# Performance work log

Hardware: AMD Instinct MI355X
Metric: run time of the kernel (lower is better)

The kernel has to match this reference:

```python
import jax, jax.numpy as jnp
import numpy as np

HIDDEN = 1024
HEADS = 16
DK = HIDDEN // HEADS  # 64
B, N = 2, 2048


def setup_inputs() -> dict:
    key = jax.random.key(0)
    ks = jax.random.split(key, 12)
    s = 0.02
    return {
        "q": jax.random.normal(ks[0], (B, N, HIDDEN), jnp.float32),
        "k": jax.random.normal(ks[1], (B, N, HIDDEN), jnp.float32),
        "v": jax.random.normal(ks[2], (B, N, HIDDEN), jnp.float32),
        "attn_bias": jax.random.normal(ks[3], (B, N, N), jnp.float32),
        "attention_mask": jnp.zeros((B, N, N), jnp.float32),
        # projection weights stored [in, out]
        "Wq": jax.random.normal(ks[4], (HIDDEN, HIDDEN), jnp.float32) * s,
        "bq": jnp.zeros((HIDDEN,), jnp.float32),
        "Wk": jax.random.normal(ks[5], (HIDDEN, HIDDEN), jnp.float32) * s,
        "bk": jnp.zeros((HIDDEN,), jnp.float32),
        "Wv": jax.random.normal(ks[6], (HIDDEN, HIDDEN), jnp.float32) * s,
        "bv": jnp.zeros((HIDDEN,), jnp.float32),
        "Wo": jax.random.normal(ks[7], (HIDDEN, HIDDEN), jnp.float32) * s,
        "bo": jnp.zeros((HIDDEN,), jnp.float32),
    }


def reference(q, k, v, attn_bias, attention_mask, Wq, bq, Wk, bk, Wv, bv, Wo, bo):
    b, n, _ = q.shape
    scale = DK ** (-0.5)
    # project and split heads: [B, H, N, Dk]
    qh = (q @ Wq + bq).reshape(b, n, HEADS, DK).transpose(0, 2, 1, 3)
    kh = (k @ Wk + bk).reshape(b, -1, HEADS, DK).transpose(0, 2, 1, 3)
    vh = (v @ Wv + bv).reshape(b, -1, HEADS, DK).transpose(0, 2, 1, 3)
    # scaled scores + additive bias/mask broadcast over heads: [B, H, N, N]
    scores = jnp.einsum('bhnd,bhmd->bhnm', qh * scale, kh)
    scores = scores + attn_bias[:, None, :, :] + attention_mask[:, None, :, :]
    probs = jax.nn.softmax(scores, axis=-1)  # dropout is identity at inference
    ctx = jnp.einsum('bhnm,bhmd->bhnd', probs, vh)
    ctx = ctx.transpose(0, 2, 1, 3).reshape(b, n, HEADS * DK)
    return ctx @ Wo + bo
```

## Files before the change

kernel.cpp:

```cpp
#include <hip/hip_runtime.h>
#include <hip/hip_bf16.h>

#define HIDDEN 1024
#define NHEADS 16
#define DKH   64
#define BATCH 2
#define SEQ   2048
#define MTOT  (BATCH*SEQ)

using bf16x8 = __attribute__((ext_vector_type(8))) short;
using f32x4  = __attribute__((ext_vector_type(4))) float;
using u16x4  = __attribute__((ext_vector_type(4))) unsigned short;

__device__ __forceinline__ unsigned short f2bf(float f) {
    union { __hip_bfloat16 h; unsigned short u; } v;
    v.h = __float2bfloat16(f);
    return v.u;
}

__device__ __forceinline__ float asfloat(unsigned int u) {
    union { unsigned int u; float f; } v; v.u = u; return v.f;
}

__device__ __forceinline__ float fexp2(float x) {
#if __has_builtin(__builtin_amdgcn_exp2f)
    return __builtin_amdgcn_exp2f(x);
#else
    return exp2f(x);
#endif
}

__device__ __forceinline__ void gload16(const unsigned short* g, unsigned short* l) {
    __builtin_amdgcn_global_load_lds((const __attribute__((address_space(1))) void*)g,
                                     (__attribute__((address_space(3))) void*)l, 16, 0, 0);
}

#define L2E 1.44269504088896340736f

__global__ __launch_bounds__(256) void cvt_qkv(const float4* __restrict__ q,
                                               const float4* __restrict__ k,
                                               const float4* __restrict__ v,
                                               u16x4* __restrict__ out) {
    int i = blockIdx.x * 256 + threadIdx.x;
    const int per = MTOT * HIDDEN / 4;
    const float4* src; int t;
    if (i < per)            { src = q; t = 0; }
    else if (i < 2 * per)   { src = k; t = 1; }
    else                    { src = v; t = 2; }
    float4 f = src[i - t * per];
    u16x4 o; o.x = f2bf(f.x); o.y = f2bf(f.y); o.z = f2bf(f.z); o.w = f2bf(f.w);
    out[i] = o;
}

__global__ __launch_bounds__(256) void cvt_w(const float* __restrict__ Wq,
                                             const float* __restrict__ Wk,
                                             const float* __restrict__ Wv,
                                             const float* __restrict__ Wo,
                                             unsigned short* __restrict__ wt) {
    __shared__ float tile[64][65];
    const float* W = (blockIdx.z == 0) ? Wq : (blockIdx.z == 1) ? Wk : (blockIdx.z == 2) ? Wv : Wo;
    unsigned short* out = wt + (size_t)blockIdx.z * HIDDEN * HIDDEN;
    int kb = blockIdx.x * 64, nb = blockIdx.y * 64;
    int t = threadIdx.x;
    #pragma unroll
    for (int i = 0; i < 16; i++) {
        int idx = i * 256 + t; int r = idx >> 6, c = idx & 63;
        tile[r][c] = W[(size_t)(kb + r) * HIDDEN + nb + c];
    }
    __syncthreads();
    #pragma unroll
    for (int i = 0; i < 16; i++) {
        int idx = i * 256 + t; int n = idx >> 6, kk = idx & 63;
        out[(size_t)(nb + n) * HIDDEN + kb + kk] = f2bf(tile[kk][n]);
    }
}

__global__ __launch_bounds__(256) void combine_bias_t(const float* __restrict__ bias,
                                                      const float* __restrict__ mask,
                                                      unsigned short* __restrict__ out) {
    const int kvb = blockIdx.x, qt = blockIdx.y, b = blockIdx.z;
    const int t = threadIdx.x;
    const int q = t >> 2, kvc = (t & 3) * 8;
    const float* bp = bias + ((size_t)b * SEQ + qt * 64 + q) * SEQ + kvb * 32 + kvc;
    const float* mp = mask + ((size_t)b * SEQ + qt * 64 + q) * SEQ + kvb * 32 + kvc;
    float4 b0 = *(const float4*)bp, b1 = *(const float4*)(bp + 4);
    float4 m0 = *(const float4*)mp, m1 = *(const float4*)(mp + 4);
    union { bf16x8 v; __hip_bfloat162 hh[4]; } o;
    o.hh[0] = __float22bfloat162_rn(make_float2((b0.x + m0.x) * L2E, (b0.y + m0.y) * L2E));
    o.hh[1] = __float22bfloat162_rn(make_float2((b0.z + m0.z) * L2E, (b0.w + m0.w) * L2E));
    o.hh[2] = __float22bfloat162_rn(make_float2((b1.x + m1.x) * L2E, (b1.y + m1.y) * L2E));
    o.hh[3] = __float22bfloat162_rn(make_float2((b1.z + m1.z) * L2E, (b1.w + m1.w) * L2E));
    *(bf16x8*)(out + ((size_t)(b * 32 + qt) * 64 + kvb) * 2048 + t * 8) = o.v;
}

__device__ __forceinline__ void gemm_core_128(const unsigned short* __restrict__ X,
                                              const unsigned short* __restrict__ Wt,
                                              unsigned short* smem,
                                              int mbase, int nbase, f32x4 acc[4][4]) {
    const int tid = threadIdx.x, w = tid >> 6, ln = tid & 63;
    const int qr = (w >> 1) * 64, qc = (w & 1) * 64;
    const int g = ln >> 4, c16 = ln & 15;
    #pragma unroll
    for (int rt = 0; rt < 4; rt++)
        #pragma unroll
        for (int ct = 0; ct < 4; ct++) acc[rt][ct] = (f32x4){0.f, 0.f, 0.f, 0.f};

    for (int kk = 0; kk < HIDDEN; kk += 64) {
        __syncthreads();
        #pragma unroll
        for (int pass = 0; pass < 4; pass++) {
            int L = pass * 256 + tid;
            int r = L >> 3, c = (L & 7) ^ (r & 7);
            gload16(X  + (size_t)(mbase + r) * HIDDEN + kk + c * 8,
                    smem + (size_t)(pass * 256 + w * 64) * 8);
            gload16(Wt + (size_t)(nbase + r) * HIDDEN + kk + c * 8,
                    smem + 8192 + (size_t)(pass * 256 + w * 64) * 8);
        }
        __syncthreads();
        #pragma unroll
        for (int ks = 0; ks < 2; ks++) {
            bf16x8 af[4], bfr[4];
            #pragma unroll
            for (int rt = 0; rt < 4; rt++) {
                int r = qr + rt * 16 + c16;
                int ch = (g + ks * 4) ^ (r & 7);
                af[rt] = *(const bf16x8*)(smem + (size_t)(r * 8 + ch) * 8);
            }
            #pragma unroll
            for (int ct = 0; ct < 4; ct++) {
                int n = qc + ct * 16 + c16;
                int ch = (g + ks * 4) ^ (n & 7);
                bfr[ct] = *(const bf16x8*)(smem + 8192 + (size_t)(n * 8 + ch) * 8);
            }
            #pragma unroll
            for (int rt = 0; rt < 4; rt++)
                #pragma unroll
                for (int ct = 0; ct < 4; ct++)
                    acc[rt][ct] = __builtin_amdgcn_mfma_f32_16x16x32_bf16(af[rt], bfr[ct], acc[rt][ct], 0, 0, 0);
        }
    }
    __syncthreads();
}

__global__ __launch_bounds__(256, 2) void proj_gemm(const unsigned short* __restrict__ Xall,
                                                    const unsigned short* __restrict__ Wtall,
                                                    const float* __restrict__ bq,
                                                    const float* __restrict__ bk,
                                                    const float* __restrict__ bv,
                                                    unsigned short* __restrict__ qh,
                                                    unsigned short* __restrict__ khp,
                                                    unsigned short* __restrict__ vtt) {
    __shared__ __align__(16) unsigned short smem[18432];
    const int z = blockIdx.z;
    const unsigned short* X  = Xall  + (size_t)z * MTOT * HIDDEN;
    const unsigned short* Wt = Wtall + (size_t)z * HIDDEN * HIDDEN;
    const float* bias = (z == 0) ? bq : (z == 1) ? bk : bv;
    const int mbase = blockIdx.x * 128, nbase = blockIdx.y * 128;
    const int tid = threadIdx.x, w = tid >> 6, ln = tid & 63;
    const int qr = (w >> 1) * 64, qc = (w & 1) * 64;
    const int g = ln >> 4, c16 = ln & 15;

    f32x4 acc[4][4];
    gemm_core_128(X, Wt, smem, mbase, nbase, acc);

    const float scale = (z == 0) ? (0.125f * L2E) : 1.0f;
    float bias_v[4];
    #pragma unroll
    for (int ct = 0; ct < 4; ct++) bias_v[ct] = bias[nbase + qc + ct * 16 + c16];

    unsigned short* eld = smem + w * 4608;
    #pragma unroll
    for (int rt = 0; rt < 4; rt++)
        #pragma unroll
        for (int ct = 0; ct < 4; ct++)
            #pragma unroll
            for (int r4 = 0; r4 < 4; r4++) {
                int row_l = rt * 16 + g * 4 + r4;
                int col_l = ct * 16 + c16;
                float val = (acc[rt][ct][r4] + bias_v[ct]) * scale;
                if (z == 2) eld[col_l * 72 + row_l] = f2bf(val);
                else        eld[row_l * 72 + col_l] = f2bf(val);
            }
    __syncthreads();

    const int b = mbase >> 11;
    const int pos0 = (mbase & 2047) + qr;
    const int h = (nbase + qc) >> 6;
    const int bh = b * NHEADS + h;
    if (z == 0) {
        const int row8 = ln >> 3, col8 = (ln & 7) * 8;
        unsigned short* dst0 = qh + ((size_t)bh * SEQ + pos0) * DKH;
        #pragma unroll
        for (int j = 0; j < 8; j++) {
            int row = j * 8 + row8;
            *(bf16x8*)(dst0 + row * 64 + col8) = *(const bf16x8*)&eld[row * 72 + col8];
        }
    } else if (z == 1) {
        unsigned short* base = khp + ((size_t)bh * 64 + (pos0 >> 5)) * 2048;
        const int x = ln >> 2;
        #pragma unroll
        for (int j = 0; j < 8; j++) {
            int kvl  = (x >> 2) * 8 + (j & 1) * 4 + (x & 3);
            int row  = (j >> 2) * 32 + kvl;
            int dcol = ((j >> 1) & 1) * 32 + (ln & 3) * 8;
            *(bf16x8*)(base + j * 512 + ln * 8) = *(const bf16x8*)&eld[row * 72 + dcol];
        }
    } else {
        unsigned short* base = vtt + ((size_t)bh * 64 + (pos0 >> 5)) * 2048;
        #pragma unroll
        for (int j = 0; j < 8; j++) {
            int o = j * 512 + ln * 8;
            int tloc = o >> 11;
            int dl = (o & 2047) >> 5;
            int kvo = (ln & 3) * 8;
            *(bf16x8*)(base + o) = *(const bf16x8*)&eld[dl * 72 + tloc * 32 + kvo];
        }
    }
}

__global__ __launch_bounds__(256, 4) void attn(const unsigned short* __restrict__ qh,
                                               const unsigned short* __restrict__ khp,
                                               const unsigned short* __restrict__ vtt,
                                               const unsigned short* __restrict__ biasc,
                                               unsigned short* __restrict__ ctx) {
    __shared__ __align__(16) float red[2][2048];
    __shared__ float lred[2][32];
    __shared__ __align__(16) unsigned short tr[2][32][72];
    const int tid = threadIdx.x;
    const int w = tid >> 6, ln = tid & 63;
    const int quad = ln >> 4, c16 = ln & 15;
    const int qg = w & 1, kg = w >> 1;
    const int bid = blockIdx.x;
    const int xcd = bid & 7, s = bid >> 3;
    const int pair = xcd * 8 + (s >> 4);
    const int h = s & 15;
    const int b = pair >> 5, qt = pair & 31;
    const int bh = b * NHEADS + h;

    bf16x8 qf[2][2];
    #pragma unroll
    for (int qsub = 0; qsub < 2; qsub++) {
        const unsigned short* qp = qh + ((size_t)bh * SEQ + qt * 64 + qg * 32 + qsub * 16 + c16) * DKH + quad * 8;
        qf[qsub][0] = *(const bf16x8*)qp;
        qf[qsub][1] = *(const bf16x8*)(qp + 32);
    }

    const unsigned short* kbase = khp + (size_t)bh * 64 * 2048 + kg * 32 * 2048;
    const unsigned short* vbase = vtt + (size_t)bh * 64 * 2048 + kg * 32 * 2048;
    const unsigned short* bbase = biasc + (size_t)(b * 32 + qt) * 64 * 2048
                                + kg * 32 * 2048 + qg * 32 * 32;

    f32x4 accv[4][2];
    #pragma unroll
    for (int dt = 0; dt < 4; dt++)
        #pragma unroll
        for (int qsub = 0; qsub < 2; qsub++) accv[dt][qsub] = (f32x4){0.f, 0.f, 0.f, 0.f};
    float lacc[2] = {0.f, 0.f};

    const int lofsK = c16 * 32 + quad * 8;
    for (int j = 0; j < 32; j++) {
        const unsigned short* kt_ = kbase + j * 2048;
        const unsigned short* vt_ = vbase + j * 2048;
        const unsigned short* bt_ = bbase + j * 2048;

        bf16x8 kf[2][2];
        #pragma unroll
        for (int ks = 0; ks < 2; ks++)
            #pragma unroll
            for (int kvs = 0; kvs < 2; kvs++)
                kf[ks][kvs] = *(const bf16x8*)(kt_ + ks * 1024 + kvs * 512 + lofsK);
        bf16x8 vf[4];
        #pragma unroll
        for (int dt = 0; dt < 4; dt++)
            vf[dt] = *(const bf16x8*)(vt_ + (dt * 16 + c16) * 32 + quad * 8);
        bf16x8 braw[2];
        #pragma unroll
        for (int qsub = 0; qsub < 2; qsub++)
            braw[qsub] = *(const bf16x8*)(bt_ + (qsub * 16 + c16) * 32 + quad * 8);

        #pragma unroll
        for (int qsub = 0; qsub < 2; qsub++) {
            const unsigned int* bd = (const unsigned int*)&braw[qsub];
            f32x4 s0, s1;
            s0[0] = asfloat(bd[0] << 16); s0[1] = asfloat(bd[0] & 0xFFFF0000u);
            s0[2] = asfloat(bd[1] << 16); s0[3] = asfloat(bd[1] & 0xFFFF0000u);
            s1[0] = asfloat(bd[2] << 16); s1[1] = asfloat(bd[2] & 0xFFFF0000u);
            s1[2] = asfloat(bd[3] << 16); s1[3] = asfloat(bd[3] & 0xFFFF0000u);
            s0 = __builtin_amdgcn_mfma_f32_16x16x32_bf16(kf[0][0], qf[qsub][0], s0, 0, 0, 0);
            s0 = __builtin_amdgcn_mfma_f32_16x16x32_bf16(kf[1][0], qf[qsub][1], s0, 0, 0, 0);
            s1 = __builtin_amdgcn_mfma_f32_16x16x32_bf16(kf[0][1], qf[qsub][0], s1, 0, 0, 0);
            s1 = __builtin_amdgcn_mfma_f32_16x16x32_bf16(kf[1][1], qf[qsub][1], s1, 0, 0, 0);
            #pragma unroll
            for (int r = 0; r < 4; r++) { s0[r] = fexp2(s0[r]); s1[r] = fexp2(s1[r]); }
            lacc[qsub] += ((s0[0] + s0[1]) + (s0[2] + s0[3]))
                        + ((s1[0] + s1[1]) + (s1[2] + s1[3]));
            union { bf16x8 v; __hip_bfloat162 hh[4]; } pu;
            pu.hh[0] = __float22bfloat162_rn(make_float2(s0[0], s0[1]));
            pu.hh[1] = __float22bfloat162_rn(make_float2(s0[2], s0[3]));
            pu.hh[2] = __float22bfloat162_rn(make_float2(s1[0], s1[1]));
            pu.hh[3] = __float22bfloat162_rn(make_float2(s1[2], s1[3]));
            #pragma unroll
            for (int dt = 0; dt < 4; dt++)
                accv[dt][qsub] = __builtin_amdgcn_mfma_f32_16x16x32_bf16(vf[dt], pu.v, accv[dt][qsub], 0, 0, 0);
        }
    }

    if (kg == 1) {
        float* dst = red[qg];
        #pragma unroll
        for (int dt = 0; dt < 4; dt++)
            #pragma unroll
            for (int qsub = 0; qsub < 2; qsub++)
                *(f32x4*)(dst + (dt * 2 + qsub) * 256 + ln * 4) = accv[dt][qsub];
        #pragma unroll
        for (int qsub = 0; qsub < 2; qsub++) {
            float l = lacc[qsub];
            l += __shfl_xor(l, 16);
            l += __shfl_xor(l, 32);
            if (quad == 0) lred[qg][qsub * 16 + c16] = l;
        }
    }
    __syncthreads();
    if (kg == 0) {
        float inv[2];
        #pragma unroll
        for (int qsub = 0; qsub < 2; qsub++) {
            float l = lacc[qsub];
            l += __shfl_xor(l, 16);
            l += __shfl_xor(l, 32);
            l += lred[qg][qsub * 16 + c16];
            inv[qsub] = 1.0f / l;
        }
        #pragma unroll
        for (int dt = 0; dt < 4; dt++)
            #pragma unroll
            for (int qsub = 0; qsub < 2; qsub++) {
                accv[dt][qsub] += *(const f32x4*)(red[qg] + (dt * 2 + qsub) * 256 + ln * 4);
                #pragma unroll
                for (int r = 0; r < 4; r += 2) {
                    union { __hip_bfloat162 hh; unsigned int u; } pk;
                    pk.hh = __float22bfloat162_rn(make_float2(accv[dt][qsub][r] * inv[qsub],
                                                             accv[dt][qsub][r + 1] * inv[qsub]));
                    *(unsigned int*)&tr[qg][qsub * 16 + c16][dt * 16 + quad * 4 + r] = pk.u;
                }
            }
    }
    __syncthreads();
    if (kg == 0) {
        int q = ln >> 1, dc = (ln & 1) * 32;
        const unsigned short* srcp = &tr[qg][q][dc];
        unsigned short* dstp = ctx + ((size_t)b * SEQ + qt * 64 + qg * 32 + q) * HIDDEN + h * 64 + dc;
        *(bf16x8*)dstp        = *(const bf16x8*)srcp;
        *(bf16x8*)(dstp + 8)  = *(const bf16x8*)(srcp + 8);
        *(bf16x8*)(dstp + 16) = *(const bf16x8*)(srcp + 16);
        *(bf16x8*)(dstp + 24) = *(const bf16x8*)(srcp + 24);
    }
}

__global__ __launch_bounds__(256, 2) void outproj(const unsigned short* __restrict__ X,
                                                  const unsigned short* __restrict__ Wt,
                                                  const float* __restrict__ bo,
                                                  float* __restrict__ out) {
    __shared__ __align__(16) unsigned short smem[16384];
    const int mbase = blockIdx.x * 128, nbase = blockIdx.y * 128;
    const int tid = threadIdx.x, w = tid >> 6, ln = tid & 63;
    const int qr = (w >> 1) * 64, qc = (w & 1) * 64;
    const int g = ln >> 4, c16 = ln & 15;

    f32x4 acc[4][4];
    gemm_core_128(X, Wt, smem, mbase, nbase, acc);

    float bo_v[4];
    #pragma unroll
    for (int ct = 0; ct < 4; ct++) bo_v[ct] = bo[nbase + qc + ct * 16 + c16];
    #pragma unroll
    for (int rt = 0; rt < 4; rt++)
        #pragma unroll
        for (int ct = 0; ct < 4; ct++)
            #pragma unroll
            for (int r4 = 0; r4 < 4; r4++)
                out[(size_t)(mbase + qr + rt * 16 + g * 4 + r4) * HIDDEN + nbase + qc + ct * 16 + c16]
                    = acc[rt][ct][r4] + bo_v[ct];
}

extern "C" void kernel_launch(void* const* d_in, const int* in_sizes, int n_in,
                              void* d_out, int out_size, void* d_ws, size_t ws_size,
                              hipStream_t stream) {
    const float* q    = (const float*)d_in[0];
    const float* k    = (const float*)d_in[1];
    const float* v    = (const float*)d_in[2];
    const float* bias = (const float*)d_in[3];
    const float* mask = (const float*)d_in[4];
    const float* Wq   = (const float*)d_in[5];
    const float* bq   = (const float*)d_in[6];
    const float* Wk   = (const float*)d_in[7];
    const float* bk   = (const float*)d_in[8];
    const float* Wv   = (const float*)d_in[9];
    const float* bv   = (const float*)d_in[10];
    const float* Wo   = (const float*)d_in[11];
    const float* bo   = (const float*)d_in[12];

    char* ws = (char*)d_ws;
    unsigned short* qkv_bf = (unsigned short*)(ws);
    unsigned short* wt     = (unsigned short*)(ws + 25165824);
    unsigned short* qh     = (unsigned short*)(ws + 33554432);
    unsigned short* khp    = (unsigned short*)(ws + 41943040);
    unsigned short* vtt    = (unsigned short*)(ws + 50331648);
    unsigned short* ctx    = (unsigned short*)(ws + 58720256);
    unsigned short* biasc  = (unsigned short*)(ws + 67108864);

    cvt_qkv<<<12288, 256, 0, stream>>>((const float4*)q, (const float4*)k, (const float4*)v,
                                       (u16x4*)qkv_bf);
    cvt_w<<<dim3(16, 16, 4), 256, 0, stream>>>(Wq, Wk, Wv, Wo, wt);
    combine_bias_t<<<dim3(64, 32, 2), 256, 0, stream>>>(bias, mask, biasc);
    proj_gemm<<<dim3(32, 8, 3), 256, 0, stream>>>(qkv_bf, wt, bq, bk, bv, qh, khp, vtt);
    attn<<<1024, 256, 0, stream>>>(qh, khp, vtt, biasc, ctx);
    outproj<<<dim3(32, 8), 256, 0, stream>>>(ctx, wt + (size_t)3 * HIDDEN * HIDDEN, bo,
                                             (float*)d_out);
}
```

Measured before the change: 317.0 us.

## Fuse prep kernels and restructure attention to share K/V tiles via LDS

Merges the three conversion kernels (qkv cast, weight transpose, bias+mask combine) into one prep launch, which removes launch gaps. Attention now uses 512 blocks of 128 query rows, with each of four waves owning 32 rows over the full KV range. The blocks stage K/V tiles into LDS with global_load_lds, so all four waves reuse each tile instead of each loading it from global memory. The split-KV cross-wave reduction goes away, bias loads are prefetched one tile ahead, and the K/V/bias layouts are reworked to match. In exchange, occupancy drops to 2 blocks per CU, there are two barriers per tile, and the grid has fewer blocks.

```diff
diff --git a/kernel.cpp b/kernel.cpp
--- a/kernel.cpp
+++ b/kernel.cpp
@@ -37,60 +37,66 @@
 
 #define L2E 1.44269504088896340736f
 
-__global__ __launch_bounds__(256) void cvt_qkv(const float4* __restrict__ q,
-                                               const float4* __restrict__ k,
-                                               const float4* __restrict__ v,
-                                               u16x4* __restrict__ out) {
-    int i = blockIdx.x * 256 + threadIdx.x;
-    const int per = MTOT * HIDDEN / 4;
-    const float4* src; int t;
-    if (i < per)            { src = q; t = 0; }
-    else if (i < 2 * per)   { src = k; t = 1; }
-    else                    { src = v; t = 2; }
-    float4 f = src[i - t * per];
-    u16x4 o; o.x = f2bf(f.x); o.y = f2bf(f.y); o.z = f2bf(f.z); o.w = f2bf(f.w);
-    out[i] = o;
-}
-
-__global__ __launch_bounds__(256) void cvt_w(const float* __restrict__ Wq,
-                                             const float* __restrict__ Wk,
-                                             const float* __restrict__ Wv,
-                                             const float* __restrict__ Wo,
-                                             unsigned short* __restrict__ wt) {
+__global__ __launch_bounds__(256) void prep(const float4* __restrict__ q,
+                                            const float4* __restrict__ k,
+                                            const float4* __restrict__ v,
+                                            u16x4* __restrict__ qkv_bf,
+                                            const float* __restrict__ Wq,
+                                            const float* __restrict__ Wk,
+                                            const float* __restrict__ Wv,
+                                            const float* __restrict__ Wo,
+                                            unsigned short* __restrict__ wt,
+                                            const float* __restrict__ bias,
+                                            const float* __restrict__ mask,
+                                            unsigned short* __restrict__ biasf) {
     __shared__ float tile[64][65];
-    const float* W = (blockIdx.z == 0) ? Wq : (blockIdx.z == 1) ? Wk : (blockIdx.z == 2) ? Wv : Wo;
-    unsigned short* out = wt + (size_t)blockIdx.z * HIDDEN * HIDDEN;
-    int kb = blockIdx.x * 64, nb = blockIdx.y * 64;
-    int t = threadIdx.x;
-    #pragma unroll
-    for (int i = 0; i < 16; i++) {
-        int idx = i * 256 + t; int r = idx >> 6, c = idx & 63;
-        tile[r][c] = W[(size_t)(kb + r) * HIDDEN + nb + c];
-    }
-    __syncthreads();
-    #pragma unroll
-    for (int i = 0; i < 16; i++) {
-        int idx = i * 256 + t; int n = idx >> 6, kk = idx & 63;
-        out[(size_t)(nb + n) * HIDDEN + kb + kk] = f2bf(tile[kk][n]);
-    }
-}
-
-__global__ __launch_bounds__(256) void combine_bias_t(const float* __restrict__ bias,
-                                                      const float* __restrict__ mask,
-                                                      unsigned short* __restrict__ out) {
-    const int kvb = blockIdx.x, qt = blockIdx.y, b = blockIdx.z;
-    const int t = threadIdx.x;
-    const int q = t >> 2, kvc = (t & 3) * 8;
-    const float* bp = bias + ((size_t)b * SEQ + qt * 64 + q) * SEQ + kvb * 32 + kvc;
-    const float* mp = mask + ((size_t)b * SEQ + qt * 64 + q) * SEQ + kvb * 32 + kvc;
-    float4 b0 = *(const float4*)bp, b1 = *(const float4*)(bp + 4);
-    float4 m0 = *(const float4*)mp, m1 = *(const float4*)(mp + 4);
-    union { bf16x8 v; __hip_bfloat162 hh[4]; } o;
-    o.hh[0] = __float22bfloat162_rn(make_float2((b0.x + m0.x) * L2E, (b0.y + m0.y) * L2E));
-    o.hh[1] = __float22bfloat162_rn(make_float2((b0.z + m0.z) * L2E, (b0.w + m0.w) * L2E));
-    o.hh[2] = __float22bfloat162_rn(make_float2((b1.x + m1.x) * L2E, (b1.y + m1.y) * L2E));
-    o.hh[3] = __float22bfloat162_rn(make_float2((b1.z + m1.z) * L2E, (b1.w + m1.w) * L2E));
-    *(bf16x8*)(out + ((size_t)(b * 32 + qt) * 64 + kvb) * 2048 + t * 8) = o.v;
+    const int bid = blockIdx.x, t = threadIdx.x;
+    if (bid < 12288) {
+        int i = bid * 256 + t;
+        const int per = MTOT * HIDDEN / 4;
+        const float4* src; int tt;
+        if (i < per)            { src = q; tt = 0; }
+        else if (i < 2 * per)   { src = k; tt = 1; }
+        else                    { src = v; tt = 2; }
+        float4 f = src[i - tt * per];
+        u16x4 o; o.x = f2bf(f.x); o.y = f2bf(f.y); o.z = f2bf(f.z); o.w = f2bf(f.w);
+        qkv_bf[i] = o;
+    } else if (bid < 13312) {
+        int r = bid - 12288;
+        const int z = r >> 8; r &= 255;
+        const int kb = (r >> 4) * 64, nb = (r & 15) * 64;
+        const float* W = (z == 0) ? Wq : (z == 1) ? Wk : (z == 2) ? Wv : Wo;
+        unsigned short* out = wt + (size_t)z * HIDDEN * HIDDEN;
+        #pragma unroll
+        for (int i = 0; i < 16; i++) {
+            int idx = i * 256 + t; int rr = idx >> 6, c = idx & 63;
+            tile[rr][c] = W[(size_t)(kb + rr) * HIDDEN + nb + c];
+        }
+        __syncthreads();
+        #pragma unroll
+        for (int i = 0; i < 16; i++) {
+            int idx = i * 256 + t; int n = idx >> 6, kk = idx & 63;
+            out[(size_t)(nb + n) * HIDDEN + kb + kk] = f2bf(tile[kk][n]);
+        }
+    } else {
+        const int cb = bid - 13312;
+        const int tblk = cb & 15, g = (cb >> 4) & 127, b = cb >> 11;
+        const int tsub = t >> 6, ln = t & 63;
+        const int c16 = ln & 15, quad = ln >> 4;
+        const int tt_ = tblk * 4 + tsub;
+        const int qq = g * 16 + c16;
+        const int kv0 = tt_ * 32 + quad * 8;
+        const float* bp = bias + ((size_t)b * SEQ + qq) * SEQ + kv0;
+        const float* mp = mask + ((size_t)b * SEQ + qq) * SEQ + kv0;
+        float4 b0 = *(const float4*)bp, b1 = *(const float4*)(bp + 4);
+        float4 m0 = *(const float4*)mp, m1 = *(const float4*)(mp + 4);
+        union { bf16x8 v; __hip_bfloat162 hh[4]; } o;
+        o.hh[0] = __float22bfloat162_rn(make_float2((b0.x + m0.x) * L2E, (b0.y + m0.y) * L2E));
+        o.hh[1] = __float22bfloat162_rn(make_float2((b0.z + m0.z) * L2E, (b0.w + m0.w) * L2E));
+        o.hh[2] = __float22bfloat162_rn(make_float2((b1.x + m1.x) * L2E, (b1.y + m1.y) * L2E));
+        o.hh[3] = __float22bfloat162_rn(make_float2((b1.z + m1.z) * L2E, (b1.w + m1.w) * L2E));
+        *(bf16x8*)(biasf + (((size_t)b * 128 + g) * 64 + tt_) * 512 + ln * 8) = o.v;
+    }
 }
 
 __device__ __forceinline__ void gemm_core_128(const unsigned short* __restrict__ X,
@@ -148,8 +154,8 @@
                                                     const float* __restrict__ bk,
                                                     const float* __restrict__ bv,
                                                     unsigned short* __restrict__ qh,
-                                                    unsigned short* __restrict__ khp,
-                                                    unsigned short* __restrict__ vtt) {
+                                                    unsigned short* __restrict__ khs,
+                                                    unsigned short* __restrict__ vts) {
     __shared__ __align__(16) unsigned short smem[18432];
     const int z = blockIdx.z;
     const unsigned short* X  = Xall  + (size_t)z * MTOT * HIDDEN;
@@ -196,59 +202,52 @@
             *(bf16x8*)(dst0 + row * 64 + col8) = *(const bf16x8*)&eld[row * 72 + col8];
         }
     } else if (z == 1) {
-        unsigned short* base = khp + ((size_t)bh * 64 + (pos0 >> 5)) * 2048;
-        const int x = ln >> 2;
+        unsigned short* base = khs + ((size_t)bh * 64 + (pos0 >> 5)) * 2048;
+        const int kvp = (c16 >> 2) * 8 + (c16 & 3);
         #pragma unroll
         for (int j = 0; j < 8; j++) {
-            int kvl  = (x >> 2) * 8 + (j & 1) * 4 + (x & 3);
-            int row  = (j >> 2) * 32 + kvl;
-            int dcol = ((j >> 1) & 1) * 32 + (ln & 3) * 8;
-            *(bf16x8*)(base + j * 512 + ln * 8) = *(const bf16x8*)&eld[row * 72 + dcol];
+            int tloc = j >> 2, ks = (j >> 1) & 1, kvs = j & 1;
+            int kvl = tloc * 32 + kvp + kvs * 4;
+            *(bf16x8*)(base + tloc * 2048 + ks * 1024 + kvs * 512 + ln * 8)
+                = *(const bf16x8*)&eld[kvl * 72 + ks * 32 + g * 8];
         }
     } else {
-        unsigned short* base = vtt + ((size_t)bh * 64 + (pos0 >> 5)) * 2048;
+        unsigned short* base = vts + ((size_t)bh * 64 + (pos0 >> 5)) * 2048;
         #pragma unroll
         for (int j = 0; j < 8; j++) {
-            int o = j * 512 + ln * 8;
-            int tloc = o >> 11;
-            int dl = (o & 2047) >> 5;
-            int kvo = (ln & 3) * 8;
-            *(bf16x8*)(base + o) = *(const bf16x8*)&eld[dl * 72 + tloc * 32 + kvo];
-        }
-    }
-}
-
-__global__ __launch_bounds__(256, 4) void attn(const unsigned short* __restrict__ qh,
-                                               const unsigned short* __restrict__ khp,
-                                               const unsigned short* __restrict__ vtt,
-                                               const unsigned short* __restrict__ biasc,
+            int tloc = j >> 2, dt = j & 3;
+            *(bf16x8*)(base + tloc * 2048 + dt * 512 + ln * 8)
+                = *(const bf16x8*)&eld[(dt * 16 + c16) * 72 + tloc * 32 + g * 8];
+        }
+    }
+}
+
+__global__ __launch_bounds__(256, 2) void attn(const unsigned short* __restrict__ qh,
+                                               const unsigned short* __restrict__ khs,
+                                               const unsigned short* __restrict__ vts,
+                                               const unsigned short* __restrict__ biasf,
                                                unsigned short* __restrict__ ctx) {
-    __shared__ __align__(16) float red[2][2048];
-    __shared__ float lred[2][32];
-    __shared__ __align__(16) unsigned short tr[2][32][72];
-    const int tid = threadIdx.x;
-    const int w = tid >> 6, ln = tid & 63;
+    __shared__ __align__(16) unsigned short smem[16384];
+    const int tid = threadIdx.x, w = tid >> 6, ln = tid & 63;
     const int quad = ln >> 4, c16 = ln & 15;
-    const int qg = w & 1, kg = w >> 1;
     const int bid = blockIdx.x;
-    const int xcd = bid & 7, s = bid >> 3;
-    const int pair = xcd * 8 + (s >> 4);
-    const int h = s & 15;
-    const int b = pair >> 5, qt = pair & 31;
-    const int bh = b * NHEADS + h;
+    const int xcd = bid & 7, jj = bid >> 3;
+    const int bh = xcd * 4 + (jj >> 4);
+    const int qb = jj & 15;
+    const int b = bh >> 4, h = bh & 15;
 
     bf16x8 qf[2][2];
     #pragma unroll
     for (int qsub = 0; qsub < 2; qsub++) {
-        const unsigned short* qp = qh + ((size_t)bh * SEQ + qt * 64 + qg * 32 + qsub * 16 + c16) * DKH + quad * 8;
+        const unsigned short* qp = qh + ((size_t)bh * SEQ + qb * 128 + w * 32 + qsub * 16 + c16) * DKH + quad * 8;
         qf[qsub][0] = *(const bf16x8*)qp;
         qf[qsub][1] = *(const bf16x8*)(qp + 32);
     }
 
-    const unsigned short* kbase = khp + (size_t)bh * 64 * 2048 + kg * 32 * 2048;
-    const unsigned short* vbase = vtt + (size_t)bh * 64 * 2048 + kg * 32 * 2048;
-    const unsigned short* bbase = biasc + (size_t)(b * 32 + qt) * 64 * 2048
-                                + kg * 32 * 2048 + qg * 32 * 32;
+    const unsigned short* kT = khs + (size_t)bh * 131072;
+    const unsigned short* vT = vts + (size_t)bh * 131072;
+    const unsigned short* bb0 = biasf + (((size_t)b * 128 + qb * 8 + w * 2) * 64) * 512 + ln * 8;
+    const unsigned short* bb1 = bb0 + 32768;
 
     f32x4 accv[4][2];
     #pragma unroll
@@ -257,104 +256,104 @@
         for (int qsub = 0; qsub < 2; qsub++) accv[dt][qsub] = (f32x4){0.f, 0.f, 0.f, 0.f};
     float lacc[2] = {0.f, 0.f};
 
-    const int lofsK = c16 * 32 + quad * 8;
-    for (int j = 0; j < 32; j++) {
-        const unsigned short* kt_ = kbase + j * 2048;
-        const unsigned short* vt_ = vbase + j * 2048;
-        const unsigned short* bt_ = bbase + j * 2048;
-
-        bf16x8 kf[2][2];
-        #pragma unroll
-        for (int ks = 0; ks < 2; ks++)
-            #pragma unroll
-            for (int kvs = 0; kvs < 2; kvs++)
-                kf[ks][kvs] = *(const bf16x8*)(kt_ + ks * 1024 + kvs * 512 + lofsK);
-        bf16x8 vf[4];
-        #pragma unroll
-        for (int dt = 0; dt < 4; dt++)
-            vf[dt] = *(const bf16x8*)(vt_ + (dt * 16 + c16) * 32 + quad * 8);
-        bf16x8 braw[2];
+    bf16x8 bcur[2][4];
+    #pragma unroll
+    for (int j = 0; j < 4; j++) {
+        bcur[0][j] = *(const bf16x8*)(bb0 + j * 512);
+        bcur[1][j] = *(const bf16x8*)(bb1 + j * 512);
+    }
+
+    for (int T = 0; T < 16; T++) {
+        __syncthreads();
+        {
+            const unsigned short* ksrc = kT + T * 8192 + w * 512 + ln * 8;
+            const unsigned short* vsrc = vT + T * 8192 + w * 512 + ln * 8;
+            unsigned short* lk = smem + w * 512;
+            unsigned short* lv = smem + 8192 + w * 512;
+            #pragma unroll
+            for (int p = 0; p < 4; p++) {
+                gload16(ksrc + p * 2048, lk + p * 2048);
+                gload16(vsrc + p * 2048, lv + p * 2048);
+            }
+        }
+        bf16x8 bnext[2][4];
+        {
+            const int Tn = (T < 15) ? T + 1 : 15;
+            #pragma unroll
+            for (int j = 0; j < 4; j++) {
+                bnext[0][j] = *(const bf16x8*)(bb0 + (Tn * 4 + j) * 512);
+                bnext[1][j] = *(const bf16x8*)(bb1 + (Tn * 4 + j) * 512);
+            }
+        }
+        __syncthreads();
+        #pragma unroll
+        for (int j = 0; j < 4; j++) {
+            bf16x8 kf00 = *(const bf16x8*)(smem + j * 2048 + ln * 8);
+            bf16x8 kf01 = *(const bf16x8*)(smem + j * 2048 + 512 + ln * 8);
+            bf16x8 kf10 = *(const bf16x8*)(smem + j * 2048 + 1024 + ln * 8);
+            bf16x8 kf11 = *(const bf16x8*)(smem + j * 2048 + 1536 + ln * 8);
+            bf16x8 vf[4];
+            #pragma unroll
+            for (int dt = 0; dt < 4; dt++)
+                vf[dt] = *(const bf16x8*)(smem + 8192 + j * 2048 + dt * 512 + ln * 8);
+            #pragma unroll
+            for (int qsub = 0; qsub < 2; qsub++) {
+                const unsigned int* bd = (const unsigned int*)&bcur[qsub][j];
+                f32x4 s0, s1;
+                s0[0] = asfloat(bd[0] << 16); s0[1] = asfloat(bd[0] & 0xFFFF0000u);
+                s0[2] = asfloat(bd[1] << 16); s0[3] = asfloat(bd[1] & 0xFFFF0000u);
+                s1[0] = asfloat(bd[2] << 16); s1[1] = asfloat(bd[2] & 0xFFFF0000u);
+                s1[2] = asfloat(bd[3] << 16); s1[3] = asfloat(bd[3] & 0xFFFF0000u);
+                s0 = __builtin_amdgcn_mfma_f32_16x16x32_bf16(kf00, qf[qsub][0], s0, 0, 0, 0);
+                s0 = __builtin_amdgcn_mfma_f32_16x16x32_bf16(kf10, qf[qsub][1], s0, 0, 0, 0);
+                s1 = __builtin_amdgcn_mfma_f32_16x16x32_bf16(kf01, qf[qsub][0], s1, 0, 0, 0);
+                s1 = __builtin_amdgcn_mfma_f32_16x16x32_bf16(kf11, qf[qsub][1], s1, 0, 0, 0);
+                #pragma unroll
+                for (int r = 0; r < 4; r++) { s0[r] = fexp2(s0[r]); s1[r] = fexp2(s1[r]); }
+                lacc[qsub] += ((s0[0] + s0[1]) + (s0[2] + s0[3]))
+                            + ((s1[0] + s1[1]) + (s1[2] + s1[3]));
+                union { bf16x8 v; __hip_bfloat162 hh[4]; } pu;
+                pu.hh[0] = __float22bfloat162_rn(make_float2(s0[0], s0[1]));
+                pu.hh[1] = __float22bfloat162_rn(make_float2(s0[2], s0[3]));
+                pu.hh[2] = __float22bfloat162_rn(make_float2(s1[0], s1[1]));
+                pu.hh[3] = __float22bfloat162_rn(make_float2(s1[2], s1[3]));
+                #pragma unroll
+                for (int dt = 0; dt < 4; dt++)
+                    accv[dt][qsub] = __builtin_amdgcn_mfma_f32_16x16x32_bf16(vf[dt], pu.v, accv[dt][qsub], 0, 0, 0);
+            }
+            bcur[0][j] = bnext[0][j];
+            bcur[1][j] = bnext[1][j];
+        }
+    }
+
+    float inv[2];
+    #pragma unroll
+    for (int qsub = 0; qsub < 2; qsub++) {
+        float l = lacc[qsub];
+        l += __shfl_xor(l, 16);
+        l += __shfl_xor(l, 32);
+        inv[qsub] = 1.0f / l;
+    }
+    __syncthreads();
+    unsigned short* ot = smem + w * 2304;
+    #pragma unroll
+    for (int dt = 0; dt < 4; dt++)
         #pragma unroll
         for (int qsub = 0; qsub < 2; qsub++)
-            braw[qsub] = *(const bf16x8*)(bt_ + (qsub * 16 + c16) * 32 + quad * 8);
-
-        #pragma unroll
-        for (int qsub = 0; qsub < 2; qsub++) {
-            const unsigned int* bd = (const unsigned int*)&braw[qsub];
-            f32x4 s0, s1;
-            s0[0] = asfloat(bd[0] << 16); s0[1] = asfloat(bd[0] & 0xFFFF0000u);
-            s0[2] = asfloat(bd[1] << 16); s0[3] = asfloat(bd[1] & 0xFFFF0000u);
-            s1[0] = asfloat(bd[2] << 16); s1[1] = asfloat(bd[2] & 0xFFFF0000u);
-            s1[2] = asfloat(bd[3] << 16); s1[3] = asfloat(bd[3] & 0xFFFF0000u);
-            s0 = __builtin_amdgcn_mfma_f32_16x16x32_bf16(kf[0][0], qf[qsub][0], s0, 0, 0, 0);
-            s0 = __builtin_amdgcn_mfma_f32_16x16x32_bf16(kf[1][0], qf[qsub][1], s0, 0, 0, 0);
-            s1 = __builtin_amdgcn_mfma_f32_16x16x32_bf16(kf[0][1], qf[qsub][0], s1, 0, 0, 0);
-            s1 = __builtin_amdgcn_mfma_f32_16x16x32_bf16(kf[1][1], qf[qsub][1], s1, 0, 0, 0);
-            #pragma unroll
-            for (int r = 0; r < 4; r++) { s0[r] = fexp2(s0[r]); s1[r] = fexp2(s1[r]); }
-            lacc[qsub] += ((s0[0] + s0[1]) + (s0[2] + s0[3]))
-                        + ((s1[0] + s1[1]) + (s1[2] + s1[3]));
-            union { bf16x8 v; __hip_bfloat162 hh[4]; } pu;
-            pu.hh[0] = __float22bfloat162_rn(make_float2(s0[0], s0[1]));
-            pu.hh[1] = __float22bfloat162_rn(make_float2(s0[2], s0[3]));
-            pu.hh[2] = __float22bfloat162_rn(make_float2(s1[0], s1[1]));
-            pu.hh[3] = __float22bfloat162_rn(make_float2(s1[2], s1[3]));
-            #pragma unroll
-            for (int dt = 0; dt < 4; dt++)
-                accv[dt][qsub] = __builtin_amdgcn_mfma_f32_16x16x32_bf16(vf[dt], pu.v, accv[dt][qsub], 0, 0, 0);
-        }
-    }
-
-    if (kg == 1) {
-        float* dst = red[qg];
-        #pragma unroll
-        for (int dt = 0; dt < 4; dt++)
-            #pragma unroll
-            for (int qsub = 0; qsub < 2; qsub++)
-                *(f32x4*)(dst + (dt * 2 + qsub) * 256 + ln * 4) = accv[dt][qsub];
-        #pragma unroll
-        for (int qsub = 0; qsub < 2; qsub++) {
-            float l = lacc[qsub];
-            l += __shfl_xor(l, 16);
-            l += __shfl_xor(l, 32);
-            if (quad == 0) lred[qg][qsub * 16 + c16] = l;
-        }
-    }
-    __syncthreads();
-    if (kg == 0) {
-        float inv[2];
-        #pragma unroll
-        for (int qsub = 0; qsub < 2; qsub++) {
-            float l = lacc[qsub];
-            l += __shfl_xor(l, 16);
-            l += __shfl_xor(l, 32);
-            l += lred[qg][qsub * 16 + c16];
-            inv[qsub] = 1.0f / l;
-        }
-        #pragma unroll
-        for (int dt = 0; dt < 4; dt++)
-            #pragma unroll
-            for (int qsub = 0; qsub < 2; qsub++) {
-                accv[dt][qsub] += *(const f32x4*)(red[qg] + (dt * 2 + qsub) * 256 + ln * 4);
-                #pragma unroll
-                for (int r = 0; r < 4; r += 2) {
-                    union { __hip_bfloat162 hh; unsigned int u; } pk;
-                    pk.hh = __float22bfloat162_rn(make_float2(accv[dt][qsub][r] * inv[qsub],
-                                                             accv[dt][qsub][r + 1] * inv[qsub]));
-                    *(unsigned int*)&tr[qg][qsub * 16 + c16][dt * 16 + quad * 4 + r] = pk.u;
-                }
-            }
-    }
-    __syncthreads();
-    if (kg == 0) {
-        int q = ln >> 1, dc = (ln & 1) * 32;
-        const unsigned short* srcp = &tr[qg][q][dc];
-        unsigned short* dstp = ctx + ((size_t)b * SEQ + qt * 64 + qg * 32 + q) * HIDDEN + h * 64 + dc;
-        *(bf16x8*)dstp        = *(const bf16x8*)srcp;
-        *(bf16x8*)(dstp + 8)  = *(const bf16x8*)(srcp + 8);
-        *(bf16x8*)(dstp + 16) = *(const bf16x8*)(srcp + 16);
-        *(bf16x8*)(dstp + 24) = *(const bf16x8*)(srcp + 24);
-    }
+            #pragma unroll
+            for (int r = 0; r < 4; r += 2) {
+                union { __hip_bfloat162 hh; unsigned int u; } pk;
+                pk.hh = __float22bfloat162_rn(make_float2(accv[dt][qsub][r] * inv[qsub],
+                                                         accv[dt][qsub][r + 1] * inv[qsub]));
+                *(unsigned int*)&ot[(qsub * 16 + c16) * 72 + dt * 16 + quad * 4 + r] = pk.u;
+            }
+    const int qrow2 = ln >> 1, half = ln & 1;
+    const unsigned short* srcp = ot + qrow2 * 72 + half * 32;
+    unsigned short* dstp = ctx + ((size_t)b * SEQ + qb * 128 + w * 32 + qrow2) * HIDDEN
+                         + h * 64 + half * 32;
+    #pragma unroll
+    for (int kk = 0; kk < 4; kk++)
+        *(bf16x8*)(dstp + kk * 8) = *(const bf16x8*)(srcp + kk * 8);
 }
 
 __global__ __launch_bounds__(256, 2) void outproj(const unsigned short* __restrict__ X,
@@ -404,17 +403,15 @@
     unsigned short* qkv_bf = (unsigned short*)(ws);
     unsigned short* wt     = (unsigned short*)(ws + 25165824);
     unsigned short* qh     = (unsigned short*)(ws + 33554432);
-    unsigned short* khp    = (unsigned short*)(ws + 41943040);
-    unsigned short* vtt    = (unsigned short*)(ws + 50331648);
+    unsigned short* khs    = (unsigned short*)(ws + 41943040);
+    unsigned short* vts    = (unsigned short*)(ws + 50331648);
     unsigned short* ctx    = (unsigned short*)(ws + 58720256);
-    unsigned short* biasc  = (unsigned short*)(ws + 67108864);
-
-    cvt_qkv<<<12288, 256, 0, stream>>>((const float4*)q, (const float4*)k, (const float4*)v,
-                                       (u16x4*)qkv_bf);
-    cvt_w<<<dim3(16, 16, 4), 256, 0, stream>>>(Wq, Wk, Wv, Wo, wt);
-    combine_bias_t<<<dim3(64, 32, 2), 256, 0, stream>>>(bias, mask, biasc);
-    proj_gemm<<<dim3(32, 8, 3), 256, 0, stream>>>(qkv_bf, wt, bq, bk, bv, qh, khp, vtt);
-    attn<<<1024, 256, 0, stream>>>(qh, khp, vtt, biasc, ctx);
+    unsigned short* biasf  = (unsigned short*)(ws + 67108864);
+
+    prep<<<17408, 256, 0, stream>>>((const float4*)q, (const float4*)k, (const float4*)v,
+                                    (u16x4*)qkv_bf, Wq, Wk, Wv, Wo, wt, bias, mask, biasf);
+    proj_gemm<<<dim3(32, 8, 3), 256, 0, stream>>>(qkv_bf, wt, bq, bk, bv, qh, khs, vts);
+    attn<<<512, 256, 0, stream>>>(qh, khs, vts, biasf, ctx);
     outproj<<<dim3(32, 8), 256, 0, stream>>>(ctx, wt + (size_t)3 * HIDDEN * HIDDEN, bo,
                                              (float*)d_out);
 }
```

New measurement: 277.5 us. -12.5%, faster.
